# Kernel tuning notes

Measured on AMD Instinct MI355X. Metric: run time of the kernel, lower is better.

## Reference

```python
import jax, jax.numpy as jnp
import numpy as np

# Synthetic layered DAG: 8 node-layers of width N -> 7 masked dense layers.
B = 4096        # batch
N = 2048        # nodes per DAG layer (= in_features = out_features)
DEPTH = 7       # number of weight layers (len(L) - 1)
DENSITY = 0.25  # fraction of predecessor edges present (mask sparsity)


def setup_inputs() -> dict:
    key = jax.random.key(0)
    kx, kw, km = jax.random.split(key, 3)
    x = jax.random.normal(kx, (B, N), dtype=jnp.float32)
    # Mask M: [DEPTH, N+1, N]; random 0/1 edges, last row (bias) all ones.
    m = (jax.random.uniform(km, (DEPTH, N + 1, N)) < DENSITY).astype(jnp.float32)
    M = m.at[:, -1, :].set(1.0)
    # Kaiming-uniform per column: bound = 1/sqrt(nnz_j) (torch code's init),
    # nonzero only at masked positions (W initialized to zeros elsewhere).
    nnz = jnp.maximum(M.sum(axis=1, keepdims=True), 1.0)  # [DEPTH,1,N]
    u = jax.random.uniform(kw, (DEPTH, N + 1, N), minval=-1.0, maxval=1.0)
    W = (u / jnp.sqrt(nnz)) * M
    return {"x": x, "W": W, "M": M}


def reference(x, W, M):
    # activations buffer semantics collapse to a per-layer chain because each
    # layer's preds are exactly the previous DAG layer; sinks = last layer.
    def step(acts, wm):
        w, m = wm  # [N+1, N] each
        h = jnp.concatenate(
            [acts, jnp.ones((acts.shape[0], 1), acts.dtype)], axis=1)  # [B, N+1]
        acts = jax.nn.relu(h @ (m * w))  # masked dense matmul + ReLU
        return acts, None

    out, _ = jax.lax.scan(step, x, (W, M))
    return out  # [B, N] activations of sink nodes
```

## Files before the change

### kernel.cpp

```cpp
#include <hip/hip_runtime.h>
#include <hip/hip_bf16.h>

typedef __bf16 bf16_t;
typedef __bf16 v8bf __attribute__((ext_vector_type(8)));
typedef float  v4f  __attribute__((ext_vector_type(4)));

#define B_ROWS 4096
#define N_COLS 2048
#define K_FULL 2049
#define K_PAD  2112
#define DEPTH  7

#define BM 128
#define BN 128
#define BK 64

__global__ __launch_bounds__(256) void wt_kernel(const float* __restrict__ W,
                                                 bf16_t* __restrict__ Wt) {
  __shared__ float tile[32][33];
  const int l  = blockIdx.z;
  const int k0 = blockIdx.x * 32;
  const int n0 = blockIdx.y * 32;
  const int tx = threadIdx.x;
  const int ty = threadIdx.y;
  const float* Wl = W + (size_t)l * K_FULL * N_COLS;
#pragma unroll
  for (int r = 0; r < 4; ++r) {
    const int k = k0 + ty + r * 8;
    float v = 0.0f;
    if (k < K_FULL) v = Wl[(size_t)k * N_COLS + n0 + tx];
    tile[ty + r * 8][tx] = v;
  }
  __syncthreads();
  bf16_t* Wtl = Wt + (size_t)l * N_COLS * K_PAD;
#pragma unroll
  for (int r = 0; r < 4; ++r) {
    const int n = n0 + ty + r * 8;
    const int k = k0 + tx;
    Wtl[(size_t)n * K_PAD + k] = (bf16_t)tile[tx][ty + r * 8];
  }
}

__global__ __launch_bounds__(256) void init_kernel(const float* __restrict__ x,
                                                   bf16_t* __restrict__ A0,
                                                   bf16_t* __restrict__ A1) {
  const int c = blockIdx.x * 256 + threadIdx.x;
  const int r = blockIdx.y;
  if (c >= K_PAD) return;
  bf16_t v;
  if (c < N_COLS)      v = (bf16_t)x[(size_t)r * N_COLS + c];
  else if (c == N_COLS) v = (bf16_t)1.0f;
  else                  v = (bf16_t)0.0f;
  A0[(size_t)r * K_PAD + c] = v;
  if (c >= N_COLS) A1[(size_t)r * K_PAD + c] = v;
}

__global__ __launch_bounds__(256, 2) void gemm_kernel(
    const bf16_t* __restrict__ A, const bf16_t* __restrict__ Bt,
    bf16_t* __restrict__ Cn, float* __restrict__ Co) {
  __shared__ __align__(16) bf16_t As[BM * BK];
  __shared__ __align__(16) bf16_t Bs[BN * BK];

  const int tid  = threadIdx.x;
  const int wave = tid >> 6;
  const int lane = tid & 63;
  const int m0 = blockIdx.y * BM;
  const int n0 = blockIdx.x * BN;
  const int wm = (wave & 1) * 64;
  const int wn = (wave >> 1) * 64;
  const int quad = lane >> 4;
  const int l16  = lane & 15;

  int srow[4], scol[4];
#pragma unroll
  for (int c = 0; c < 4; ++c) {
    const int gran = wave * 256 + c * 64 + lane;
    srow[c] = gran >> 3;
    scol[c] = ((gran & 7) ^ (srow[c] & 7)) << 3;
  }

  v4f acc[4][4] = {};

  for (int kt = 0; kt < K_PAD / BK; ++kt) {
    const int kbase = kt * BK;
    __syncthreads();
#pragma unroll
    for (int c = 0; c < 4; ++c) {
      const bf16_t* g = A + (size_t)(m0 + srow[c]) * K_PAD + kbase + scol[c];
      __builtin_amdgcn_global_load_lds(
          (const __attribute__((address_space(1))) void*)g,
          (__attribute__((address_space(3))) void*)((char*)As + wave * 4096 + c * 1024),
          16, 0, 0);
    }
#pragma unroll
    for (int c = 0; c < 4; ++c) {
      const bf16_t* g = Bt + (size_t)(n0 + srow[c]) * K_PAD + kbase + scol[c];
      __builtin_amdgcn_global_load_lds(
          (const __attribute__((address_space(1))) void*)g,
          (__attribute__((address_space(3))) void*)((char*)Bs + wave * 4096 + c * 1024),
          16, 0, 0);
    }
    __syncthreads();

#pragma unroll
    for (int ks = 0; ks < 2; ++ks) {
      v8bf af[4], bfr[4];
#pragma unroll
      for (int i = 0; i < 4; ++i) {
        const int arow = wm + i * 16 + l16;
        const int kg   = ks * 4 + quad;
        af[i] = *(const v8bf*)&As[arow * BK + ((kg ^ (arow & 7)) << 3)];
        const int brow = wn + i * 16 + l16;
        bfr[i] = *(const v8bf*)&Bs[brow * BK + ((kg ^ (brow & 7)) << 3)];
      }
#pragma unroll
      for (int i = 0; i < 4; ++i)
#pragma unroll
        for (int j = 0; j < 4; ++j)
          acc[i][j] = __builtin_amdgcn_mfma_f32_16x16x32_bf16(af[i], bfr[j],
                                                              acc[i][j], 0, 0, 0);
    }
  }

#pragma unroll
  for (int i = 0; i < 4; ++i) {
#pragma unroll
    for (int j = 0; j < 4; ++j) {
#pragma unroll
      for (int r = 0; r < 4; ++r) {
        float v = acc[i][j][r];
        v = v > 0.0f ? v : 0.0f;
        const int row = m0 + wm + i * 16 + quad * 4 + r;
        const int col = n0 + wn + j * 16 + l16;
        if (Co) Co[(size_t)row * N_COLS + col] = v;
        else    Cn[(size_t)row * K_PAD + col] = (bf16_t)v;
      }
    }
  }
}

extern "C" void kernel_launch(void* const* d_in, const int* in_sizes, int n_in,
                              void* d_out, int out_size, void* d_ws, size_t ws_size,
                              hipStream_t stream) {
  const float* x = (const float*)d_in[0];
  const float* W = (const float*)d_in[1];
  float* out = (float*)d_out;

  char* ws = (char*)d_ws;
  const size_t wtBytes = (size_t)DEPTH * N_COLS * K_PAD * sizeof(bf16_t);
  const size_t aBytes  = (size_t)B_ROWS * K_PAD * sizeof(bf16_t);
  bf16_t* Wt = (bf16_t*)ws;
  bf16_t* A0 = (bf16_t*)(ws + wtBytes);
  bf16_t* A1 = (bf16_t*)(ws + wtBytes + aBytes);

  wt_kernel<<<dim3(K_PAD / 32, N_COLS / 32, DEPTH), dim3(32, 8), 0, stream>>>(W, Wt);
  init_kernel<<<dim3((K_PAD + 255) / 256, B_ROWS), 256, 0, stream>>>(x, A0, A1);

  bf16_t* bufs[2] = {A0, A1};
  for (int l = 0; l < DEPTH; ++l) {
    const bf16_t* Ain = bufs[l & 1];
    bf16_t* Aout      = bufs[(l + 1) & 1];
    const bf16_t* Bl  = Wt + (size_t)l * N_COLS * K_PAD;
    const bool last   = (l == DEPTH - 1);
    gemm_kernel<<<dim3(N_COLS / BN, B_ROWS / BM), 256, 0, stream>>>(
        Ain, Bl, last ? nullptr : Aout, last ? out : nullptr);
  }
}
```

Baseline: 545.1 us.

## Double-buffer LDS tiles in GEMM and vectorize weight transpose and init kernels

The GEMM main loop now keeps two LDS buffers and issues the global-to-LDS loads for the next K tile before computing the current one. It waits with explicit vmcnt counters and raw s_barrier, so memory latency overlaps with MFMA work. The weight transpose and input init kernels switch to float4 loads and 4-wide bf16 stores, and the transpose uses larger 64x64 tiles. The pipelining doubles LDS per block, which may reduce occupancy, and it relies on hand-written wait counts.

```diff
diff --git a/kernel.cpp b/kernel.cpp
--- a/kernel.cpp
+++ b/kernel.cpp
@@ -3,6 +3,7 @@
 
 typedef __bf16 bf16_t;
 typedef __bf16 v8bf __attribute__((ext_vector_type(8)));
+typedef __bf16 v4bf __attribute__((ext_vector_type(4)));
 typedef float  v4f  __attribute__((ext_vector_type(4)));
 
 #define B_ROWS 4096
@@ -14,52 +15,65 @@
 #define BM 128
 #define BN 128
 #define BK 64
+#define NT (K_PAD / BK)
 
 __global__ __launch_bounds__(256) void wt_kernel(const float* __restrict__ W,
                                                  bf16_t* __restrict__ Wt) {
-  __shared__ float tile[32][33];
+  __shared__ float t[64][65];
   const int l  = blockIdx.z;
-  const int k0 = blockIdx.x * 32;
-  const int n0 = blockIdx.y * 32;
-  const int tx = threadIdx.x;
-  const int ty = threadIdx.y;
+  const int k0 = blockIdx.x * 64;
+  const int n0 = blockIdx.y * 64;
+  const int tid = threadIdx.x;
+  const int r  = tid >> 4;
+  const int c4 = (tid & 15) * 4;
   const float* Wl = W + (size_t)l * K_FULL * N_COLS;
 #pragma unroll
-  for (int r = 0; r < 4; ++r) {
-    const int k = k0 + ty + r * 8;
-    float v = 0.0f;
-    if (k < K_FULL) v = Wl[(size_t)k * N_COLS + n0 + tx];
-    tile[ty + r * 8][tx] = v;
+  for (int it = 0; it < 4; ++it) {
+    const int k = k0 + r + it * 16;
+    float4 v = make_float4(0.f, 0.f, 0.f, 0.f);
+    if (k < K_FULL) v = *(const float4*)&Wl[(size_t)k * N_COLS + n0 + c4];
+    t[c4 + 0][r + it * 16] = v.x;
+    t[c4 + 1][r + it * 16] = v.y;
+    t[c4 + 2][r + it * 16] = v.z;
+    t[c4 + 3][r + it * 16] = v.w;
   }
   __syncthreads();
   bf16_t* Wtl = Wt + (size_t)l * N_COLS * K_PAD;
 #pragma unroll
-  for (int r = 0; r < 4; ++r) {
-    const int n = n0 + ty + r * 8;
-    const int k = k0 + tx;
-    Wtl[(size_t)n * K_PAD + k] = (bf16_t)tile[tx][ty + r * 8];
+  for (int it = 0; it < 4; ++it) {
+    const int n = r + it * 16;
+    v4bf o;
+    o[0] = (bf16_t)t[n][c4 + 0];
+    o[1] = (bf16_t)t[n][c4 + 1];
+    o[2] = (bf16_t)t[n][c4 + 2];
+    o[3] = (bf16_t)t[n][c4 + 3];
+    *(v4bf*)&Wtl[(size_t)(n0 + n) * K_PAD + k0 + c4] = o;
   }
 }
 
 __global__ __launch_bounds__(256) void init_kernel(const float* __restrict__ x,
                                                    bf16_t* __restrict__ A0,
                                                    bf16_t* __restrict__ A1) {
-  const int c = blockIdx.x * 256 + threadIdx.x;
-  const int r = blockIdx.y;
-  if (c >= K_PAD) return;
-  bf16_t v;
-  if (c < N_COLS)      v = (bf16_t)x[(size_t)r * N_COLS + c];
-  else if (c == N_COLS) v = (bf16_t)1.0f;
-  else                  v = (bf16_t)0.0f;
-  A0[(size_t)r * K_PAD + c] = v;
-  if (c >= N_COLS) A1[(size_t)r * K_PAD + c] = v;
+  const int c4 = (blockIdx.x * 256 + threadIdx.x) * 4;
+  const int r  = blockIdx.y;
+  if (c4 >= K_PAD) return;
+  v4bf o;
+  if (c4 < N_COLS) {
+    const float4 v = *(const float4*)&x[(size_t)r * N_COLS + c4];
+    o[0] = (bf16_t)v.x; o[1] = (bf16_t)v.y; o[2] = (bf16_t)v.z; o[3] = (bf16_t)v.w;
+  } else {
+    o[0] = (bf16_t)(c4 == N_COLS ? 1.0f : 0.0f);
+    o[1] = (bf16_t)0.0f; o[2] = (bf16_t)0.0f; o[3] = (bf16_t)0.0f;
+  }
+  *(v4bf*)&A0[(size_t)r * K_PAD + c4] = o;
+  if (c4 >= N_COLS) *(v4bf*)&A1[(size_t)r * K_PAD + c4] = o;
 }
 
 __global__ __launch_bounds__(256, 2) void gemm_kernel(
     const bf16_t* __restrict__ A, const bf16_t* __restrict__ Bt,
     bf16_t* __restrict__ Cn, float* __restrict__ Co) {
-  __shared__ __align__(16) bf16_t As[BM * BK];
-  __shared__ __align__(16) bf16_t Bs[BN * BK];
+  __shared__ __align__(16) bf16_t As[2][BM * BK];
+  __shared__ __align__(16) bf16_t Bs[2][BN * BK];
 
   const int tid  = threadIdx.x;
   const int wave = tid >> 6;
@@ -79,29 +93,50 @@
     scol[c] = ((gran & 7) ^ (srow[c] & 7)) << 3;
   }
 
+  const size_t arow_off[4] = {
+      (size_t)(m0 + srow[0]) * K_PAD + scol[0],
+      (size_t)(m0 + srow[1]) * K_PAD + scol[1],
+      (size_t)(m0 + srow[2]) * K_PAD + scol[2],
+      (size_t)(m0 + srow[3]) * K_PAD + scol[3]};
+  const size_t brow_off[4] = {
+      (size_t)(n0 + srow[0]) * K_PAD + scol[0],
+      (size_t)(n0 + srow[1]) * K_PAD + scol[1],
+      (size_t)(n0 + srow[2]) * K_PAD + scol[2],
+      (size_t)(n0 + srow[3]) * K_PAD + scol[3]};
+
+  auto issue = [&](int kt, int buf) {
+    const int kbase = kt * BK;
+    char* asb = (char*)&As[buf][0] + wave * 4096;
+    char* bsb = (char*)&Bs[buf][0] + wave * 4096;
+#pragma unroll
+    for (int c = 0; c < 4; ++c) {
+      __builtin_amdgcn_global_load_lds(
+          (const __attribute__((address_space(1))) void*)(A + arow_off[c] + kbase),
+          (__attribute__((address_space(3))) void*)(asb + c * 1024), 16, 0, 0);
+    }
+#pragma unroll
+    for (int c = 0; c < 4; ++c) {
+      __builtin_amdgcn_global_load_lds(
+          (const __attribute__((address_space(1))) void*)(Bt + brow_off[c] + kbase),
+          (__attribute__((address_space(3))) void*)(bsb + c * 1024), 16, 0, 0);
+    }
+  };
+
   v4f acc[4][4] = {};
 
-  for (int kt = 0; kt < K_PAD / BK; ++kt) {
-    const int kbase = kt * BK;
-    __syncthreads();
-#pragma unroll
-    for (int c = 0; c < 4; ++c) {
-      const bf16_t* g = A + (size_t)(m0 + srow[c]) * K_PAD + kbase + scol[c];
-      __builtin_amdgcn_global_load_lds(
-          (const __attribute__((address_space(1))) void*)g,
-          (__attribute__((address_space(3))) void*)((char*)As + wave * 4096 + c * 1024),
-          16, 0, 0);
-    }
-#pragma unroll
-    for (int c = 0; c < 4; ++c) {
-      const bf16_t* g = Bt + (size_t)(n0 + srow[c]) * K_PAD + kbase + scol[c];
-      __builtin_amdgcn_global_load_lds(
-          (const __attribute__((address_space(1))) void*)g,
-          (__attribute__((address_space(3))) void*)((char*)Bs + wave * 4096 + c * 1024),
-          16, 0, 0);
-    }
-    __syncthreads();
-
+  issue(0, 0);
+  for (int kt = 0; kt < NT; ++kt) {
+    const int cur = kt & 1;
+    if (kt + 1 < NT) {
+      issue(kt + 1, cur ^ 1);
+      asm volatile("s_waitcnt vmcnt(8)" ::: "memory");
+    } else {
+      asm volatile("s_waitcnt vmcnt(0)" ::: "memory");
+    }
+    asm volatile("s_barrier" ::: "memory");
+
+    const bf16_t* as = &As[cur][0];
+    const bf16_t* bs = &Bs[cur][0];
 #pragma unroll
     for (int ks = 0; ks < 2; ++ks) {
       v8bf af[4], bfr[4];
@@ -109,9 +144,9 @@
       for (int i = 0; i < 4; ++i) {
         const int arow = wm + i * 16 + l16;
         const int kg   = ks * 4 + quad;
-        af[i] = *(const v8bf*)&As[arow * BK + ((kg ^ (arow & 7)) << 3)];
+        af[i] = *(const v8bf*)&as[arow * BK + ((kg ^ (arow & 7)) << 3)];
         const int brow = wn + i * 16 + l16;
-        bfr[i] = *(const v8bf*)&Bs[brow * BK + ((kg ^ (brow & 7)) << 3)];
+        bfr[i] = *(const v8bf*)&bs[brow * BK + ((kg ^ (brow & 7)) << 3)];
       }
 #pragma unroll
       for (int i = 0; i < 4; ++i)
@@ -120,6 +155,7 @@
           acc[i][j] = __builtin_amdgcn_mfma_f32_16x16x32_bf16(af[i], bfr[j],
                                                               acc[i][j], 0, 0, 0);
     }
+    asm volatile("s_barrier" ::: "memory");
   }
 
 #pragma unroll
@@ -153,8 +189,8 @@
   bf16_t* A0 = (bf16_t*)(ws + wtBytes);
   bf16_t* A1 = (bf16_t*)(ws + wtBytes + aBytes);
 
-  wt_kernel<<<dim3(K_PAD / 32, N_COLS / 32, DEPTH), dim3(32, 8), 0, stream>>>(W, Wt);
-  init_kernel<<<dim3((K_PAD + 255) / 256, B_ROWS), 256, 0, stream>>>(x, A0, A1);
+  wt_kernel<<<dim3(K_PAD / 64, N_COLS / 64, DEPTH), 256, 0, stream>>>(W, Wt);
+  init_kernel<<<dim3((K_PAD / 4 + 255) / 256, B_ROWS), 256, 0, stream>>>(x, A0, A1);
 
   bf16_t* bufs[2] = {A0, A1};
   for (int l = 0; l < DEPTH; ++l) {
```

Result: faster. 525.0 us (-3.7%).
